# Kernel optimization log

Measured on AMD Instinct MI355X. Metric: run time of the kernel, lower is better.

The kernel has to match this reference:

```python
import jax, jax.numpy as jnp
import numpy as np

N_HEADS = 16
KV_HEADS = 4
HEAD_DIM = 128
D_MODEL = N_HEADS * HEAD_DIM  # 2048
KV_DIM = KV_HEADS * HEAD_DIM  # 512
MAX_POS = 4096
ROPE_THETA = 10000.0
EPS = 1e-5


def _rope_cache(seq_len):
    # QEffMolmoRotaryEmbedding: inv_freq over head_dim, emb = cat(freqs, freqs)
    inv_freq = 1.0 / (ROPE_THETA ** (jnp.arange(0, HEAD_DIM, 2, dtype=jnp.float32) / HEAD_DIM))
    t = jnp.arange(seq_len, dtype=jnp.float32)
    freqs = jnp.outer(t, inv_freq)                      # [S, D/2]
    emb = jnp.concatenate([freqs, freqs], axis=-1)      # [S, D]
    return jnp.cos(emb), jnp.sin(emb)


def _rotate_half(x):
    # x: [B, H, T, D] -> cat(-x2, x1) with halves along last dim
    x1, x2 = jnp.split(x, 2, axis=-1)
    return jnp.concatenate([-x2, x1], axis=-1)


def _rms_norm(x, w):
    var = jnp.mean(jnp.square(x), axis=-1, keepdims=True)
    return (x * jax.lax.rsqrt(var + EPS)) * w


def setup_inputs() -> dict:
    key = jax.random.key(0)
    ks = jax.random.split(key, 8)
    B, T = 1, 2048
    q = jax.random.normal(ks[0], (B, T, D_MODEL), dtype=jnp.float32)
    k = jax.random.normal(ks[1], (B, T, KV_DIM), dtype=jnp.float32)
    v = jax.random.normal(ks[2], (B, T, KV_DIM), dtype=jnp.float32)
    # causal mask: True means masked (torch.where(mask, -10000, scores))
    attention_mask = jnp.triu(jnp.ones((T, T), dtype=bool), k=1)[None, None]  # [1,1,T,T]
    position_ids = jnp.arange(T, dtype=jnp.int32)[None, :]                    # [B,T]
    q_norm_w = jax.random.normal(ks[3], (D_MODEL,), dtype=jnp.float32) * 0.02 + 1.0
    k_norm_w = jax.random.normal(ks[4], (KV_DIM,), dtype=jnp.float32) * 0.02 + 1.0
    w_out = jax.random.normal(ks[5], (D_MODEL, D_MODEL), dtype=jnp.float32) * (D_MODEL ** -0.5)
    return {"q": q, "k": k, "v": v, "attention_mask": attention_mask,
            "position_ids": position_ids, "q_norm_w": q_norm_w,
            "k_norm_w": k_norm_w, "w_out": w_out}


def reference(q, k, v, attention_mask, position_ids, q_norm_w, k_norm_w, w_out):
    B, T, C = q.shape
    # QK-norm on flat projections
    q = _rms_norm(q, q_norm_w)
    k = _rms_norm(k, k_norm_w)
    # split heads: [B, H, T, D]
    q = q.reshape(B, T, N_HEADS, HEAD_DIM).transpose(0, 2, 1, 3)
    k = k.reshape(B, T, KV_HEADS, HEAD_DIM).transpose(0, 2, 1, 3)
    v = v.reshape(B, T, KV_HEADS, HEAD_DIM).transpose(0, 2, 1, 3)
    # RoPE (rotate_half variant)
    cos_c, sin_c = _rope_cache(MAX_POS)
    cos = cos_c[position_ids][:, None]  # [B,1,T,D]
    sin = sin_c[position_ids][:, None]
    q = q * cos + _rotate_half(q) * sin
    k = k * cos + _rotate_half(k) * sin
    # GQA expand
    rep = N_HEADS // KV_HEADS
    k = jnp.repeat(k, rep, axis=1)
    v = jnp.repeat(v, rep, axis=1)
    scale = 1.0 / np.sqrt(HEAD_DIM)
    scores = jnp.einsum('bhqd,bhkd->bhqk', q, k) * scale  # [B,H,T,T]
    scores = jnp.where(attention_mask, jnp.float32(-10000.0), scores)
    attn = jax.nn.softmax(scores.astype(jnp.float32), axis=-1).astype(q.dtype)
    out = jnp.einsum('bhqk,bhkd->bhqd', attn, v)          # [B,H,T,D]
    out = out.transpose(0, 2, 1, 3).reshape(B, T, C)
    return out @ w_out.T
```

## Files before the change

### kernel.cpp

```cpp
#include <hip/hip_runtime.h>
#include <hip/hip_bf16.h>
#include <math.h>

#define T_SEQ 2048
#define NH 16
#define KVH 4
#define HD 128
#define DM 2048
#define KVD 512

typedef short bf16x8 __attribute__((ext_vector_type(8)));
typedef float f32x4 __attribute__((ext_vector_type(4)));
typedef float f32x16 __attribute__((ext_vector_type(16)));
typedef unsigned int uint2v __attribute__((ext_vector_type(2)));

static __device__ __forceinline__ unsigned short f2bf(float f) {
    unsigned int x = __float_as_uint(f);
    x += 0x7fff + ((x >> 16) & 1);
    return (unsigned short)(x >> 16);
}
static __device__ __forceinline__ float bf2f(unsigned short u) {
    return __uint_as_float(((unsigned int)u) << 16);
}

static __device__ __forceinline__ unsigned int cvtpk(float lo, float hi) {
    unsigned int r;
    asm("v_cvt_pk_bf16_f32 %0, %1, %2" : "=v"(r) : "v"(lo), "v"(hi));
    return r;
}

static __device__ __forceinline__ f32x4 mfma16(bf16x8 a, bf16x8 b, f32x4 c) {
    return __builtin_amdgcn_mfma_f32_16x16x32_bf16(a, b, c, 0, 0, 0);
}
static __device__ __forceinline__ f32x16 mfma32(bf16x8 a, bf16x8 b, f32x16 c) {
    return __builtin_amdgcn_mfma_f32_32x32x16_bf16(a, b, c, 0, 0, 0);
}


__global__ __launch_bounds__(256) void qk_prep(
    const float* __restrict__ q, const float* __restrict__ k,
    const float* __restrict__ qw, const float* __restrict__ kw,
    const int* __restrict__ pos_ids,
    unsigned short* __restrict__ Qb, unsigned short* __restrict__ Ks) {
    __shared__ float qr[DM];
    __shared__ float kr[KVD];
    __shared__ float cosL[64], sinL[64];
    __shared__ float redq[4], redk[4];
    int t = blockIdx.x, tid = threadIdx.x;

    float qs = 0.f, ks = 0.f;
    {
        const float* qp = q + (size_t)t * DM + tid * 8;
        float4 v0 = *(const float4*)(qp);
        float4 v1 = *(const float4*)(qp + 4);
        float* dst = qr + tid * 8;
        dst[0] = v0.x; dst[1] = v0.y; dst[2] = v0.z; dst[3] = v0.w;
        dst[4] = v1.x; dst[5] = v1.y; dst[6] = v1.z; dst[7] = v1.w;
        qs = v0.x * v0.x + v0.y * v0.y + v0.z * v0.z + v0.w * v0.w +
             v1.x * v1.x + v1.y * v1.y + v1.z * v1.z + v1.w * v1.w;
        float2 kv = *(const float2*)(k + (size_t)t * KVD + tid * 2);
        kr[tid * 2] = kv.x; kr[tid * 2 + 1] = kv.y;
        ks = kv.x * kv.x + kv.y * kv.y;
    }
    if (tid < 64) {
        float pos = (float)pos_ids[t];
        float inv = powf(10000.0f, -(float)tid * (1.0f / 64.0f));
        float a = pos * inv;
        cosL[tid] = cosf(a);
        sinL[tid] = sinf(a);
    }
    for (int off = 32; off; off >>= 1) {
        qs += __shfl_down(qs, off);
        ks += __shfl_down(ks, off);
    }
    if ((tid & 63) == 0) { redq[tid >> 6] = qs; redk[tid >> 6] = ks; }
    __syncthreads();
    float qinv = rsqrtf((redq[0] + redq[1] + redq[2] + redq[3]) * (1.0f / DM) + 1e-5f);
    float kinv = rsqrtf((redk[0] + redk[1] + redk[2] + redk[3]) * (1.0f / KVD) + 1e-5f);

    {
        int base = tid * 8;
        int h = base >> 7;
        int d = base & 127;
        bool lo = d < 64;
        int i0 = d & 63;
        int pb = lo ? base + 64 : base - 64;
        #pragma unroll
        for (int j = 0; j < 8; ++j) {
            float xv = qr[base + j] * qinv * qw[base + j];
            float pv = qr[pb + j] * qinv * qw[pb + j];
            float c = cosL[i0 + j];
            float s = sinL[i0 + j];
            float o = lo ? (xv * c - pv * s) : (xv * c + pv * s);
            Qb[((size_t)h * T_SEQ + t) * HD + d + j] = f2bf(o);
        }
    }
    {
        int base = tid * 2;
        int kh = base >> 7;
        int d = base & 127;
        bool lo = d < 64;
        int i0 = d & 63;
        int pb = lo ? base + 64 : base - 64;
        int kt = t >> 5, lq = t & 31;
        #pragma unroll
        for (int j = 0; j < 2; ++j) {
            float xv = kr[base + j] * kinv * kw[base + j];
            float pv = kr[pb + j] * kinv * kw[pb + j];
            float c = cosL[i0 + j];
            float s = sinL[i0 + j];
            float o = lo ? (xv * c - pv * s) : (xv * c + pv * s);
            int dj = d + j;
            int sl = dj >> 4, hi2 = (dj >> 3) & 1, jj = dj & 7;
            size_t oi = ((((size_t)(kh * 64 + kt) * 8 + sl) * 2 + hi2) * 32 + lq) * 8 + jj;
            Ks[oi] = f2bf(o);
        }
    }
}

__global__ __launch_bounds__(256) void v_prep(const float* __restrict__ v,
                                              unsigned short* __restrict__ Vs) {
    __shared__ unsigned short tile[64][80];
    int tb = blockIdx.x;
    int cb = blockIdx.y;
    int tid = threadIdx.x;
    #pragma unroll 4
    for (int rep = 0; rep < 16; ++rep) {
        int e = rep * 256 + tid;
        int r = e >> 6;
        int c = e & 63;
        tile[c][r] = f2bf(v[(size_t)(tb * 64 + r) * KVD + cb * 64 + c]);
    }
    __syncthreads();
    #pragma unroll
    for (int rep = 0; rep < 2; ++rep) {
        int e = rep * 256 + tid;
        int cc = e >> 3, tg = e & 7;
        int cg = cb * 64 + cc;
        int kh = cg >> 7, crow = cg & 127, db = crow >> 5, lq = crow & 31;
        int t0g = tb * 64 + tg * 8;
        int kt = t0g >> 5, tr = t0g & 31, half = tr >> 4, hi2 = (tr >> 3) & 1;
        size_t o = (((((size_t)(kh * 64 + kt) * 2 + half) * 4 + db) * 2 + hi2) * 32 + lq) * 8;
        *(bf16x8*)(Vs + o) = *(const bf16x8*)(&tile[cc][tg * 8]);
    }
}

__global__ __launch_bounds__(256) void w_prep(const float* __restrict__ w,
                                              unsigned short* __restrict__ Wb) {
    size_t idx = ((size_t)blockIdx.x * 256 + threadIdx.x) * 4;
    float4 f = *(const float4*)(w + idx);
    ushort4 o;
    o.x = f2bf(f.x); o.y = f2bf(f.y); o.z = f2bf(f.z); o.w = f2bf(f.w);
    *(ushort4*)(Wb + idx) = o;
}

#define BEXP 20.0f
#define SCALE2 (0.08838834764831845f * 1.4426950408889634f)

#define ATTN_BODY(CUR, NXT)                                                        \
    do {                                                                           \
        const unsigned short* Vt_ = Vbase + (size_t)kt * 4096;                     \
        bf16x8 vb[8];                                                              \
        _Pragma("unroll") for (int x = 0; x < 8; ++x)                              \
            vb[x] = *(const bf16x8*)(Vt_ + x * 512);                               \
        if (kt + 1 < t1) {                                                         \
            const unsigned short* Kn_ = Kbase + (size_t)(kt + 1) * 4096;           \
            _Pragma("unroll") for (int x = 0; x < 8; ++x)                          \
                NXT[x] = *(const bf16x8*)(Kn_ + x * 512);                          \
        }                                                                          \
        f32x16 sa_, sb_;                                                           \
        _Pragma("unroll") for (int r = 0; r < 16; ++r) { sa_[r] = 0.f; sb_[r] = 0.f; } \
        _Pragma("unroll") for (int x = 0; x < 8; x += 2) {                         \
            sa_ = mfma32(CUR[x], qf[x], sa_);                                      \
            sb_ = mfma32(CUR[x + 1], qf[x + 1], sb_);                              \
        }                                                                          \
        float p_[16];                                                              \
        if (kt == nkt - 1) {                                                       \
            int lim = qglob - kt * 32;                                             \
            _Pragma("unroll") for (int r = 0; r < 16; ++r) {                       \
                float e_ = __builtin_amdgcn_exp2f((sa_[r] + sb_[r]) * SCALE2 - BEXP); \
                int off_ = (r & 3) + 8 * (r >> 2) + 4 * hi;                        \
                p_[r] = (off_ <= lim) ? e_ : 0.f;                                  \
                sden4[r & 3] += p_[r];                                             \
            }                                                                      \
        } else {                                                                   \
            _Pragma("unroll") for (int r = 0; r < 16; ++r) {                       \
                p_[r] = __builtin_amdgcn_exp2f((sa_[r] + sb_[r]) * SCALE2 - BEXP); \
                sden4[r & 3] += p_[r];                                             \
            }                                                                      \
        }                                                                          \
        _Pragma("unroll") for (int half = 0; half < 2; ++half) {                   \
            unsigned int a0 = cvtpk(p_[half * 8 + 0], p_[half * 8 + 1]);           \
            unsigned int a1 = cvtpk(p_[half * 8 + 2], p_[half * 8 + 3]);           \
            unsigned int b0 = cvtpk(p_[half * 8 + 4], p_[half * 8 + 5]);           \
            unsigned int b1 = cvtpk(p_[half * 8 + 6], p_[half * 8 + 7]);           \
            uint2v w0 = __builtin_amdgcn_permlane32_swap(a0, b0, false, false);    \
            uint2v w1 = __builtin_amdgcn_permlane32_swap(a1, b1, false, false);    \
            union { unsigned int u[4]; bf16x8 v; } pc;                             \
            pc.u[0] = w0[0]; pc.u[1] = w1[0]; pc.u[2] = w0[1]; pc.u[3] = w1[1];    \
            bf16x8 pf = pc.v;                                                      \
            _Pragma("unroll") for (int db = 0; db < 4; ++db)                       \
                oacc[db] = mfma32(vb[half * 4 + db], pf, oacc[db]);                \
        }                                                                          \
    } while (0)

__global__ __launch_bounds__(64) void attn_fwd11(
    const unsigned short* __restrict__ Qb, const unsigned short* __restrict__ Ks,
    const unsigned short* __restrict__ Vs,
    unsigned short* __restrict__ Opart, float* __restrict__ Lpart,
    unsigned short* __restrict__ Xo, int CHUNK) {
    int qrow = 63 - (int)blockIdx.x;
    int h = blockIdx.y;
    int seg = blockIdx.z;
    int kh = h >> 2;
    int l = threadIdx.x;
    int lq = l & 31, hi = l >> 5;
    int qglob = qrow * 32 + lq;

    int nkt = qrow + 1;
    int t0 = seg * CHUNK;
    int t1 = min(t0 + CHUNK, nkt);
    if (t0 >= t1) return;
    size_t idx = (size_t)(h * 64 + qrow) * 4 + seg;

    const unsigned short* Qh = Qb + (size_t)h * T_SEQ * HD;
    const unsigned short* Kbase = Ks + (size_t)kh * 64 * 4096 + l * 8;
    const unsigned short* Vbase = Vs + (size_t)kh * 64 * 4096 + l * 8;

    bf16x8 qf[8];
    #pragma unroll
    for (int sl = 0; sl < 8; ++sl)
        qf[sl] = *(const bf16x8*)(Qh + (size_t)qglob * HD + sl * 16 + hi * 8);

    f32x16 oacc[4];
    #pragma unroll
    for (int db = 0; db < 4; ++db)
        #pragma unroll
        for (int r = 0; r < 16; ++r) oacc[db][r] = 0.f;
    f32x4 sden4 = (f32x4){0.f, 0.f, 0.f, 0.f};

    bf16x8 kA[8], kB[8];
    {
        const unsigned short* K0 = Kbase + (size_t)t0 * 4096;
        #pragma unroll
        for (int x = 0; x < 8; ++x) kA[x] = *(const bf16x8*)(K0 + x * 512);
    }
    int kt = t0;
    while (true) {
        ATTN_BODY(kA, kB);
        if (++kt >= t1) break;
        ATTN_BODY(kB, kA);
        if (++kt >= t1) break;
    }

    float sden = (sden4[0] + sden4[1]) + (sden4[2] + sden4[3]);
    float sden_tot = sden + __shfl_xor(sden, 32);

    if (t0 == 0 && t1 == nkt) {
        float invs = 1.0f / sden_tot;
        #pragma unroll
        for (int db = 0; db < 4; ++db) {
            #pragma unroll
            for (int r = 0; r < 16; ++r) {
                int d = db * 32 + (r & 3) + 8 * (r >> 2) + 4 * hi;
                Xo[(size_t)qglob * DM + h * HD + d] = f2bf(oacc[db][r] * invs);
            }
        }
        return;
    }
    if (hi == 0) Lpart[idx * 32 + lq] = sden_tot;
    unsigned short* op = Opart + (idx << 12);
    #pragma unroll
    for (int db = 0; db < 4; ++db) {
        #pragma unroll
        for (int r = 0; r < 16; ++r) {
            int d = db * 32 + (r & 3) + 8 * (r >> 2) + 4 * hi;
            op[d * 32 + lq] = f2bf(oacc[db][r]);
        }
    }
}

__global__ __launch_bounds__(256) void attn_combine(
    const unsigned short* __restrict__ Opart, const float* __restrict__ Lpart,
    unsigned short* __restrict__ Xo, int CHUNK) {
    int qrow = CHUNK + blockIdx.x;
    int h = blockIdx.y;
    int tid = threadIdx.x;
    int nkt = qrow + 1;
    int used = (nkt + CHUNK - 1) / CHUNK;
    int base = (h * 64 + qrow) * 4;
    __shared__ float invden[32];
    if (tid < 32) {
        int q = tid;
        float den = 0.f;
        for (int s = 0; s < used; ++s) den += Lpart[(base + s) * 32 + q];
        invden[q] = 1.0f / den;
    }
    __syncthreads();
    int d = tid >> 1, q0 = (tid & 1) * 16;
    float acc[16];
    #pragma unroll
    for (int j = 0; j < 16; ++j) acc[j] = 0.f;
    for (int s = 0; s < used; ++s) {
        const unsigned short* op = Opart + ((size_t)(base + s) << 12) + d * 32 + q0;
        bf16x8 o0 = *(const bf16x8*)(op);
        bf16x8 o1 = *(const bf16x8*)(op + 8);
        #pragma unroll
        for (int j = 0; j < 8; ++j) {
            acc[j]     += bf2f((unsigned short)o0[j]);
            acc[8 + j] += bf2f((unsigned short)o1[j]);
        }
    }
    __shared__ unsigned short xo[32][136];
    #pragma unroll
    for (int j = 0; j < 16; ++j)
        xo[q0 + j][d] = f2bf(acc[j] * invden[q0 + j]);
    __syncthreads();
    int q = tid >> 3, dc = (tid & 7) * 16;
    bf16x8 v0 = *(const bf16x8*)(&xo[q][dc]);
    bf16x8 v1 = *(const bf16x8*)(&xo[q][dc + 8]);
    size_t ro = (size_t)(qrow * 32 + q) * DM + h * HD + dc;
    *(bf16x8*)(Xo + ro) = v0;
    *(bf16x8*)(Xo + ro + 8) = v1;
}

__global__ __launch_bounds__(256) void outproj2(
    const unsigned short* __restrict__ X, const unsigned short* __restrict__ Wb,
    float* __restrict__ out) {
    __shared__ unsigned short As[128][72];
    __shared__ unsigned short Bs[64][72];
    int tid = threadIdx.x;
    int w = tid >> 6, l = tid & 63;
    int lr = l & 15, lg = l >> 4;
    int wm = w >> 1, wn = w & 1;
    int id = blockIdx.x;
    int wg = (id & 7) * 64 + (id >> 3);
    int m0 = (wg & 15) * 128, n0 = (wg >> 4) * 64;

    int ar_row[4], ar_col[4], br_row[2], br_col[2];
    #pragma unroll
    for (int qd = 0; qd < 4; ++qd) {
        int c = tid + qd * 256;
        ar_row[qd] = c >> 3; ar_col[qd] = (c & 7) * 8;
    }
    #pragma unroll
    for (int qd = 0; qd < 2; ++qd) {
        int c = tid + qd * 256;
        br_row[qd] = c >> 3; br_col[qd] = (c & 7) * 8;
    }

    f32x4 acc[4][2];
    #pragma unroll
    for (int i = 0; i < 4; ++i)
        #pragma unroll
        for (int j = 0; j < 2; ++j) acc[i][j] = (f32x4){0.f, 0.f, 0.f, 0.f};

    bf16x8 ar[4], br[2];
    #pragma unroll
    for (int qd = 0; qd < 4; ++qd)
        ar[qd] = *(const bf16x8*)(X + (size_t)(m0 + ar_row[qd]) * DM + ar_col[qd]);
    #pragma unroll
    for (int qd = 0; qd < 2; ++qd)
        br[qd] = *(const bf16x8*)(Wb + (size_t)(n0 + br_row[qd]) * DM + br_col[qd]);
    #pragma unroll
    for (int qd = 0; qd < 4; ++qd)
        *(bf16x8*)(&As[ar_row[qd]][ar_col[qd]]) = ar[qd];
    #pragma unroll
    for (int qd = 0; qd < 2; ++qd)
        *(bf16x8*)(&Bs[br_row[qd]][br_col[qd]]) = br[qd];
    __syncthreads();

    for (int t = 0; t < DM / 64; ++t) {
        if (t + 1 < DM / 64) {
            int k0 = (t + 1) * 64;
            #pragma unroll
            for (int qd = 0; qd < 4; ++qd)
                ar[qd] = *(const bf16x8*)(X + (size_t)(m0 + ar_row[qd]) * DM + k0 + ar_col[qd]);
            #pragma unroll
            for (int qd = 0; qd < 2; ++qd)
                br[qd] = *(const bf16x8*)(Wb + (size_t)(n0 + br_row[qd]) * DM + k0 + br_col[qd]);
        }
        #pragma unroll
        for (int ks = 0; ks < 2; ++ks) {
            bf16x8 af[4], bfr[2];
            #pragma unroll
            for (int i = 0; i < 4; ++i)
                af[i] = *(const bf16x8*)(&As[wm * 64 + i * 16 + lr][ks * 32 + lg * 8]);
            #pragma unroll
            for (int j = 0; j < 2; ++j)
                bfr[j] = *(const bf16x8*)(&Bs[wn * 32 + j * 16 + lr][ks * 32 + lg * 8]);
            #pragma unroll
            for (int i = 0; i < 4; ++i)
                #pragma unroll
                for (int j = 0; j < 2; ++j)
                    acc[i][j] = mfma16(af[i], bfr[j], acc[i][j]);
        }
        if (t + 1 < DM / 64) {
            __syncthreads();
            #pragma unroll
            for (int qd = 0; qd < 4; ++qd)
                *(bf16x8*)(&As[ar_row[qd]][ar_col[qd]]) = ar[qd];
            #pragma unroll
            for (int qd = 0; qd < 2; ++qd)
                *(bf16x8*)(&Bs[br_row[qd]][br_col[qd]]) = br[qd];
            __syncthreads();
        }
    }
    #pragma unroll
    for (int i = 0; i < 4; ++i) {
        #pragma unroll
        for (int j = 0; j < 2; ++j) {
            #pragma unroll
            for (int r = 0; r < 4; ++r) {
                int row = m0 + wm * 64 + i * 16 + lg * 4 + r;
                int col = n0 + wn * 32 + j * 16 + lr;
                out[(size_t)row * DM + col] = acc[i][j][r];
            }
        }
    }
}

extern "C" void kernel_launch(void* const* d_in, const int* in_sizes, int n_in,
                              void* d_out, int out_size, void* d_ws, size_t ws_size,
                              hipStream_t stream) {
    const float* q = (const float*)d_in[0];
    const float* k = (const float*)d_in[1];
    const float* v = (const float*)d_in[2];
    const int* pos_ids = (const int*)d_in[4];
    const float* qw = (const float*)d_in[5];
    const float* kw = (const float*)d_in[6];
    const float* wout = (const float*)d_in[7];
    float* out = (float*)d_out;

    char* ws = (char*)d_ws;
    unsigned short* Qb = (unsigned short*)(ws + 0x100000);
    unsigned short* Ks = (unsigned short*)(ws + 0x900000);
    unsigned short* Vs = (unsigned short*)(ws + 0xB00000);
    unsigned short* Wb = (unsigned short*)(ws + 0xD00000);
    unsigned short* Xo = (unsigned short*)(ws + 0x1500000);
    float* Lpart = (float*)(ws + 0x1D00000);
    unsigned short* Opart = (unsigned short*)(ws + 0x1E00000);

    int CHUNK = (ws_size >= 0x1E00000ull + 4ull * 0x800000ull) ? 22 : 64;
    int zsegs = (CHUNK == 22) ? 3 : 1;

    qk_prep<<<T_SEQ, 256, 0, stream>>>(q, k, qw, kw, pos_ids, Qb, Ks);
    v_prep<<<dim3(T_SEQ / 64, KVD / 64), 256, 0, stream>>>(v, Vs);
    w_prep<<<(DM * DM) / (256 * 4), 256, 0, stream>>>(wout, Wb);
    attn_fwd11<<<dim3(64, NH, zsegs), 64, 0, stream>>>(Qb, Ks, Vs, Opart, Lpart, Xo, CHUNK);
    if (CHUNK == 22)
        attn_combine<<<dim3(64 - 22, NH), 256, 0, stream>>>(Opart, Lpart, Xo, CHUNK);
    outproj2<<<512, 256, 0, stream>>>(Xo, Wb, out);
}
```

Baseline: 99.93 us.

## Share K/V tiles across GQA heads via LDS with async double-buffered loads

The attention kernel now runs one 256-thread block per KV head, with four waves each handling one of the query heads in the group. Each K/V tile is loaded once into shared memory with global_load_lds, where previously each query head's wave fetched it separately from global memory. The next tile is prefetched into a double buffer. This cuts redundant global/L2 traffic by the GQA factor, but adds a __syncthreads per tile, reads operands from LDS, and launches a quarter as many blocks.

```diff
diff --git a/kernel.cpp b/kernel.cpp
--- a/kernel.cpp
+++ b/kernel.cpp
@@ -34,6 +34,13 @@
 }
 static __device__ __forceinline__ f32x16 mfma32(bf16x8 a, bf16x8 b, f32x16 c) {
     return __builtin_amdgcn_mfma_f32_32x32x16_bf16(a, b, c, 0, 0, 0);
+}
+
+static __device__ __forceinline__ void gl_lds16(const unsigned short* g, unsigned short* l) {
+    __builtin_amdgcn_global_load_lds(
+        (const __attribute__((address_space(1))) unsigned int*)g,
+        (__attribute__((address_space(3))) unsigned int*)l,
+        16, 0, 0);
 }
 
 
@@ -157,63 +164,27 @@
 #define BEXP 20.0f
 #define SCALE2 (0.08838834764831845f * 1.4426950408889634f)
 
-#define ATTN_BODY(CUR, NXT)                                                        \
+#define STAGE(B, KT)                                                               \
     do {                                                                           \
-        const unsigned short* Vt_ = Vbase + (size_t)kt * 4096;                     \
-        bf16x8 vb[8];                                                              \
-        _Pragma("unroll") for (int x = 0; x < 8; ++x)                              \
-            vb[x] = *(const bf16x8*)(Vt_ + x * 512);                               \
-        if (kt + 1 < t1) {                                                         \
-            const unsigned short* Kn_ = Kbase + (size_t)(kt + 1) * 4096;           \
-            _Pragma("unroll") for (int x = 0; x < 8; ++x)                          \
-                NXT[x] = *(const bf16x8*)(Kn_ + x * 512);                          \
-        }                                                                          \
-        f32x16 sa_, sb_;                                                           \
-        _Pragma("unroll") for (int r = 0; r < 16; ++r) { sa_[r] = 0.f; sb_[r] = 0.f; } \
-        _Pragma("unroll") for (int x = 0; x < 8; x += 2) {                         \
-            sa_ = mfma32(CUR[x], qf[x], sa_);                                      \
-            sb_ = mfma32(CUR[x + 1], qf[x + 1], sb_);                              \
-        }                                                                          \
-        float p_[16];                                                              \
-        if (kt == nkt - 1) {                                                       \
-            int lim = qglob - kt * 32;                                             \
-            _Pragma("unroll") for (int r = 0; r < 16; ++r) {                       \
-                float e_ = __builtin_amdgcn_exp2f((sa_[r] + sb_[r]) * SCALE2 - BEXP); \
-                int off_ = (r & 3) + 8 * (r >> 2) + 4 * hi;                        \
-                p_[r] = (off_ <= lim) ? e_ : 0.f;                                  \
-                sden4[r & 3] += p_[r];                                             \
-            }                                                                      \
-        } else {                                                                   \
-            _Pragma("unroll") for (int r = 0; r < 16; ++r) {                       \
-                p_[r] = __builtin_amdgcn_exp2f((sa_[r] + sb_[r]) * SCALE2 - BEXP); \
-                sden4[r & 3] += p_[r];                                             \
-            }                                                                      \
-        }                                                                          \
-        _Pragma("unroll") for (int half = 0; half < 2; ++half) {                   \
-            unsigned int a0 = cvtpk(p_[half * 8 + 0], p_[half * 8 + 1]);           \
-            unsigned int a1 = cvtpk(p_[half * 8 + 2], p_[half * 8 + 3]);           \
-            unsigned int b0 = cvtpk(p_[half * 8 + 4], p_[half * 8 + 5]);           \
-            unsigned int b1 = cvtpk(p_[half * 8 + 6], p_[half * 8 + 7]);           \
-            uint2v w0 = __builtin_amdgcn_permlane32_swap(a0, b0, false, false);    \
-            uint2v w1 = __builtin_amdgcn_permlane32_swap(a1, b1, false, false);    \
-            union { unsigned int u[4]; bf16x8 v; } pc;                             \
-            pc.u[0] = w0[0]; pc.u[1] = w1[0]; pc.u[2] = w0[1]; pc.u[3] = w1[1];    \
-            bf16x8 pf = pc.v;                                                      \
-            _Pragma("unroll") for (int db = 0; db < 4; ++db)                       \
-                oacc[db] = mfma32(vb[half * 4 + db], pf, oacc[db]);                \
-        }                                                                          \
+        const unsigned short* kg_ = Kt_g + (size_t)(KT) * 4096;                    \
+        const unsigned short* vg_ = Vt_g + (size_t)(KT) * 4096;                    \
+        gl_lds16(kg_ + w * 512 + l * 8,        &kv[B][w * 512]);                   \
+        gl_lds16(kg_ + 2048 + w * 512 + l * 8, &kv[B][2048 + w * 512]);            \
+        gl_lds16(vg_ + w * 512 + l * 8,        &kv[B][4096 + w * 512]);            \
+        gl_lds16(vg_ + 2048 + w * 512 + l * 8, &kv[B][6144 + w * 512]);            \
     } while (0)
 
-__global__ __launch_bounds__(64) void attn_fwd11(
+__global__ __launch_bounds__(256) void attn_fwd12(
     const unsigned short* __restrict__ Qb, const unsigned short* __restrict__ Ks,
     const unsigned short* __restrict__ Vs,
     unsigned short* __restrict__ Opart, float* __restrict__ Lpart,
     unsigned short* __restrict__ Xo, int CHUNK) {
     int qrow = 63 - (int)blockIdx.x;
-    int h = blockIdx.y;
+    int kh = blockIdx.y;
     int seg = blockIdx.z;
-    int kh = h >> 2;
-    int l = threadIdx.x;
+    int tid = threadIdx.x;
+    int w = tid >> 6, l = tid & 63;
+    int h = kh * 4 + w;
     int lq = l & 31, hi = l >> 5;
     int qglob = qrow * 32 + lq;
 
@@ -224,8 +195,10 @@
     size_t idx = (size_t)(h * 64 + qrow) * 4 + seg;
 
     const unsigned short* Qh = Qb + (size_t)h * T_SEQ * HD;
-    const unsigned short* Kbase = Ks + (size_t)kh * 64 * 4096 + l * 8;
-    const unsigned short* Vbase = Vs + (size_t)kh * 64 * 4096 + l * 8;
+    const unsigned short* Kt_g = Ks + (size_t)kh * 64 * 4096;
+    const unsigned short* Vt_g = Vs + (size_t)kh * 64 * 4096;
+
+    __shared__ unsigned short kv[2][8192];
 
     bf16x8 qf[8];
     #pragma unroll
@@ -239,18 +212,58 @@
         for (int r = 0; r < 16; ++r) oacc[db][r] = 0.f;
     f32x4 sden4 = (f32x4){0.f, 0.f, 0.f, 0.f};
 
-    bf16x8 kA[8], kB[8];
-    {
-        const unsigned short* K0 = Kbase + (size_t)t0 * 4096;
-        #pragma unroll
-        for (int x = 0; x < 8; ++x) kA[x] = *(const bf16x8*)(K0 + x * 512);
-    }
-    int kt = t0;
-    while (true) {
-        ATTN_BODY(kA, kB);
-        if (++kt >= t1) break;
-        ATTN_BODY(kB, kA);
-        if (++kt >= t1) break;
+    STAGE(0, t0);
+    int cur = 0;
+    for (int kt = t0; kt < t1; ++kt) {
+        __syncthreads();
+        if (kt + 1 < t1) STAGE(cur ^ 1, kt + 1);
+        const unsigned short* kl = &kv[cur][0] + l * 8;
+        const unsigned short* vl = &kv[cur][4096] + l * 8;
+        f32x16 sa, sb;
+        #pragma unroll
+        for (int r = 0; r < 16; ++r) { sa[r] = 0.f; sb[r] = 0.f; }
+        #pragma unroll
+        for (int x = 0; x < 8; x += 2) {
+            bf16x8 k0 = *(const bf16x8*)(kl + x * 512);
+            bf16x8 k1 = *(const bf16x8*)(kl + (x + 1) * 512);
+            sa = mfma32(k0, qf[x], sa);
+            sb = mfma32(k1, qf[x + 1], sb);
+        }
+        float p_[16];
+        if (kt == nkt - 1) {
+            int lim = qglob - kt * 32;
+            #pragma unroll
+            for (int r = 0; r < 16; ++r) {
+                float e_ = __builtin_amdgcn_exp2f((sa[r] + sb[r]) * SCALE2 - BEXP);
+                int off_ = (r & 3) + 8 * (r >> 2) + 4 * hi;
+                p_[r] = (off_ <= lim) ? e_ : 0.f;
+                sden4[r & 3] += p_[r];
+            }
+        } else {
+            #pragma unroll
+            for (int r = 0; r < 16; ++r) {
+                p_[r] = __builtin_amdgcn_exp2f((sa[r] + sb[r]) * SCALE2 - BEXP);
+                sden4[r & 3] += p_[r];
+            }
+        }
+        #pragma unroll
+        for (int half = 0; half < 2; ++half) {
+            unsigned int a0 = cvtpk(p_[half * 8 + 0], p_[half * 8 + 1]);
+            unsigned int a1 = cvtpk(p_[half * 8 + 2], p_[half * 8 + 3]);
+            unsigned int b0 = cvtpk(p_[half * 8 + 4], p_[half * 8 + 5]);
+            unsigned int b1 = cvtpk(p_[half * 8 + 6], p_[half * 8 + 7]);
+            uint2v w0 = __builtin_amdgcn_permlane32_swap(a0, b0, false, false);
+            uint2v w1 = __builtin_amdgcn_permlane32_swap(a1, b1, false, false);
+            union { unsigned int u[4]; bf16x8 v; } pc;
+            pc.u[0] = w0[0]; pc.u[1] = w1[0]; pc.u[2] = w0[1]; pc.u[3] = w1[1];
+            bf16x8 pf = pc.v;
+            #pragma unroll
+            for (int db = 0; db < 4; ++db) {
+                bf16x8 vf = *(const bf16x8*)(vl + (half * 4 + db) * 512);
+                oacc[db] = mfma32(vf, pf, oacc[db]);
+            }
+        }
+        cur ^= 1;
     }
 
     float sden = (sden4[0] + sden4[1]) + (sden4[2] + sden4[3]);
@@ -447,7 +460,7 @@
     qk_prep<<<T_SEQ, 256, 0, stream>>>(q, k, qw, kw, pos_ids, Qb, Ks);
     v_prep<<<dim3(T_SEQ / 64, KVD / 64), 256, 0, stream>>>(v, Vs);
     w_prep<<<(DM * DM) / (256 * 4), 256, 0, stream>>>(wout, Wb);
-    attn_fwd11<<<dim3(64, NH, zsegs), 64, 0, stream>>>(Qb, Ks, Vs, Opart, Lpart, Xo, CHUNK);
+    attn_fwd12<<<dim3(64, KVH, zsegs), 256, 0, stream>>>(Qb, Ks, Vs, Opart, Lpart, Xo, CHUNK);
     if (CHUNK == 22)
         attn_combine<<<dim3(64 - 22, NH), 256, 0, stream>>>(Opart, Lpart, Xo, CHUNK);
     outproj2<<<512, 256, 0, stream>>>(Xo, Wb, out);
```

Result: faster. 95.62 us (-4.3%).

## Share K/V tiles across GQA heads via LDS with async double-buffered loads

Applied to the files above, without the earlier changes.

The attention kernel now runs one 256-thread block per KV head, with four waves, one per query head in the group. Each K/V tile is loaded once into LDS with global_load_lds and double-buffered in pairs, instead of every head's wave reading the same K/V from global memory. The V and W conversion kernels are also merged into one launch. This cuts redundant K/V global traffic and one kernel launch, at the cost of barriers, more LDS per block (64 KB), and a quarter as many blocks, which may lower occupancy.

```diff
diff --git a/kernel.cpp b/kernel.cpp
--- a/kernel.cpp
+++ b/kernel.cpp
@@ -34,6 +34,13 @@
 }
 static __device__ __forceinline__ f32x16 mfma32(bf16x8 a, bf16x8 b, f32x16 c) {
     return __builtin_amdgcn_mfma_f32_32x32x16_bf16(a, b, c, 0, 0, 0);
+}
+
+static __device__ __forceinline__ void gl_lds16(const unsigned short* g, unsigned short* l) {
+    __builtin_amdgcn_global_load_lds(
+        (const __attribute__((address_space(1))) unsigned int*)g,
+        (__attribute__((address_space(3))) unsigned int*)l,
+        16, 0, 0);
 }
 
 
@@ -118,12 +125,24 @@
     }
 }
 
-__global__ __launch_bounds__(256) void v_prep(const float* __restrict__ v,
-                                              unsigned short* __restrict__ Vs) {
+__global__ __launch_bounds__(256) void vw_prep(const float* __restrict__ v,
+                                               unsigned short* __restrict__ Vs,
+                                               const float* __restrict__ w,
+                                               unsigned short* __restrict__ Wb) {
+    int bid = blockIdx.x;
+    int tid = threadIdx.x;
+    if (bid < 4096) {
+        size_t idx = ((size_t)bid * 256 + tid) * 4;
+        float4 f = *(const float4*)(w + idx);
+        ushort4 o;
+        o.x = f2bf(f.x); o.y = f2bf(f.y); o.z = f2bf(f.z); o.w = f2bf(f.w);
+        *(ushort4*)(Wb + idx) = o;
+        return;
+    }
     __shared__ unsigned short tile[64][80];
-    int tb = blockIdx.x;
-    int cb = blockIdx.y;
-    int tid = threadIdx.x;
+    int vb = bid - 4096;
+    int tb = vb & 31;
+    int cb = vb >> 5;
     #pragma unroll 4
     for (int rep = 0; rep < 16; ++rep) {
         int e = rep * 256 + tid;
@@ -145,47 +164,43 @@
     }
 }
 
-__global__ __launch_bounds__(256) void w_prep(const float* __restrict__ w,
-                                              unsigned short* __restrict__ Wb) {
-    size_t idx = ((size_t)blockIdx.x * 256 + threadIdx.x) * 4;
-    float4 f = *(const float4*)(w + idx);
-    ushort4 o;
-    o.x = f2bf(f.x); o.y = f2bf(f.y); o.z = f2bf(f.z); o.w = f2bf(f.w);
-    *(ushort4*)(Wb + idx) = o;
-}
-
 #define BEXP 20.0f
 #define SCALE2 (0.08838834764831845f * 1.4426950408889634f)
 
-#define ATTN_BODY(CUR, NXT)                                                        \
+#define STAGE1(B, S, KT)                                                           \
     do {                                                                           \
-        const unsigned short* Vt_ = Vbase + (size_t)kt * 4096;                     \
-        bf16x8 vb[8];                                                              \
-        _Pragma("unroll") for (int x = 0; x < 8; ++x)                              \
-            vb[x] = *(const bf16x8*)(Vt_ + x * 512);                               \
-        if (kt + 1 < t1) {                                                         \
-            const unsigned short* Kn_ = Kbase + (size_t)(kt + 1) * 4096;           \
-            _Pragma("unroll") for (int x = 0; x < 8; ++x)                          \
-                NXT[x] = *(const bf16x8*)(Kn_ + x * 512);                          \
-        }                                                                          \
-        f32x16 sa_, sb_;                                                           \
-        _Pragma("unroll") for (int r = 0; r < 16; ++r) { sa_[r] = 0.f; sb_[r] = 0.f; } \
+        const unsigned short* kg_ = Kt_g + (size_t)(KT) * 4096;                    \
+        const unsigned short* vg_ = Vt_g + (size_t)(KT) * 4096;                    \
+        gl_lds16(kg_ + w * 512 + l * 8,        &kv[B][S][w * 512]);                \
+        gl_lds16(kg_ + 2048 + w * 512 + l * 8, &kv[B][S][2048 + w * 512]);         \
+        gl_lds16(vg_ + w * 512 + l * 8,        &kv[B][S][4096 + w * 512]);         \
+        gl_lds16(vg_ + 2048 + w * 512 + l * 8, &kv[B][S][6144 + w * 512]);         \
+    } while (0)
+
+#define TILE_COMPUTE(BUF, SLOT, KT)                                                \
+    do {                                                                           \
+        const unsigned short* kl = &kv[BUF][SLOT][0] + l * 8;                      \
+        const unsigned short* vl = &kv[BUF][SLOT][4096] + l * 8;                   \
+        f32x16 sa, sb;                                                             \
+        _Pragma("unroll") for (int r = 0; r < 16; ++r) { sa[r] = 0.f; sb[r] = 0.f; } \
         _Pragma("unroll") for (int x = 0; x < 8; x += 2) {                         \
-            sa_ = mfma32(CUR[x], qf[x], sa_);                                      \
-            sb_ = mfma32(CUR[x + 1], qf[x + 1], sb_);                              \
+            bf16x8 k0 = *(const bf16x8*)(kl + x * 512);                            \
+            bf16x8 k1 = *(const bf16x8*)(kl + (x + 1) * 512);                      \
+            sa = mfma32(k0, qf[x], sa);                                            \
+            sb = mfma32(k1, qf[x + 1], sb);                                        \
         }                                                                          \
         float p_[16];                                                              \
-        if (kt == nkt - 1) {                                                       \
-            int lim = qglob - kt * 32;                                             \
+        if ((KT) == nkt - 1) {                                                     \
+            int lim = qglob - (KT) * 32;                                           \
             _Pragma("unroll") for (int r = 0; r < 16; ++r) {                       \
-                float e_ = __builtin_amdgcn_exp2f((sa_[r] + sb_[r]) * SCALE2 - BEXP); \
+                float e_ = __builtin_amdgcn_exp2f((sa[r] + sb[r]) * SCALE2 - BEXP); \
                 int off_ = (r & 3) + 8 * (r >> 2) + 4 * hi;                        \
                 p_[r] = (off_ <= lim) ? e_ : 0.f;                                  \
                 sden4[r & 3] += p_[r];                                             \
             }                                                                      \
         } else {                                                                   \
             _Pragma("unroll") for (int r = 0; r < 16; ++r) {                       \
-                p_[r] = __builtin_amdgcn_exp2f((sa_[r] + sb_[r]) * SCALE2 - BEXP); \
+                p_[r] = __builtin_amdgcn_exp2f((sa[r] + sb[r]) * SCALE2 - BEXP);   \
                 sden4[r & 3] += p_[r];                                             \
             }                                                                      \
         }                                                                          \
@@ -199,21 +214,24 @@
             union { unsigned int u[4]; bf16x8 v; } pc;                             \
             pc.u[0] = w0[0]; pc.u[1] = w1[0]; pc.u[2] = w0[1]; pc.u[3] = w1[1];    \
             bf16x8 pf = pc.v;                                                      \
-            _Pragma("unroll") for (int db = 0; db < 4; ++db)                       \
-                oacc[db] = mfma32(vb[half * 4 + db], pf, oacc[db]);                \
+            _Pragma("unroll") for (int db = 0; db < 4; ++db) {                     \
+                bf16x8 vf = *(const bf16x8*)(vl + (half * 4 + db) * 512);          \
+                oacc[db] = mfma32(vf, pf, oacc[db]);                               \
+            }                                                                      \
         }                                                                          \
     } while (0)
 
-__global__ __launch_bounds__(64) void attn_fwd11(
+__global__ __launch_bounds__(256) void attn_fwd18(
     const unsigned short* __restrict__ Qb, const unsigned short* __restrict__ Ks,
     const unsigned short* __restrict__ Vs,
     unsigned short* __restrict__ Opart, float* __restrict__ Lpart,
     unsigned short* __restrict__ Xo, int CHUNK) {
     int qrow = 63 - (int)blockIdx.x;
-    int h = blockIdx.y;
+    int kh = blockIdx.y;
     int seg = blockIdx.z;
-    int kh = h >> 2;
-    int l = threadIdx.x;
+    int tid = threadIdx.x;
+    int w = tid >> 6, l = tid & 63;
+    int h = kh * 4 + w;
     int lq = l & 31, hi = l >> 5;
     int qglob = qrow * 32 + lq;
 
@@ -224,8 +242,10 @@
     size_t idx = (size_t)(h * 64 + qrow) * 4 + seg;
 
     const unsigned short* Qh = Qb + (size_t)h * T_SEQ * HD;
-    const unsigned short* Kbase = Ks + (size_t)kh * 64 * 4096 + l * 8;
-    const unsigned short* Vbase = Vs + (size_t)kh * 64 * 4096 + l * 8;
+    const unsigned short* Kt_g = Ks + (size_t)kh * 64 * 4096;
+    const unsigned short* Vt_g = Vs + (size_t)kh * 64 * 4096;
+
+    __shared__ unsigned short kv[2][2][8192];
 
     bf16x8 qf[8];
     #pragma unroll
@@ -239,18 +259,28 @@
         for (int r = 0; r < 16; ++r) oacc[db][r] = 0.f;
     f32x4 sden4 = (f32x4){0.f, 0.f, 0.f, 0.f};
 
-    bf16x8 kA[8], kB[8];
-    {
-        const unsigned short* K0 = Kbase + (size_t)t0 * 4096;
-        #pragma unroll
-        for (int x = 0; x < 8; ++x) kA[x] = *(const bf16x8*)(K0 + x * 512);
-    }
+    int pairsEnd = t0 + ((t1 - t0) & ~1);
     int kt = t0;
-    while (true) {
-        ATTN_BODY(kA, kB);
-        if (++kt >= t1) break;
-        ATTN_BODY(kB, kA);
-        if (++kt >= t1) break;
+    int cur = 0;
+    if (kt < pairsEnd) { STAGE1(0, 0, kt); STAGE1(0, 1, kt + 1); }
+    if (kt + 2 < pairsEnd) { STAGE1(1, 0, kt + 2); STAGE1(1, 1, kt + 3); }
+    for (; kt < pairsEnd; kt += 2) {
+        bool more = (kt + 2 < pairsEnd);
+        if (more) asm volatile("s_waitcnt vmcnt(8)" ::: "memory");
+        else      asm volatile("s_waitcnt vmcnt(0)" ::: "memory");
+        __builtin_amdgcn_s_barrier();
+        TILE_COMPUTE(cur, 0, kt);
+        TILE_COMPUTE(cur, 1, kt + 1);
+        asm volatile("s_waitcnt lgkmcnt(0)" ::: "memory");
+        __builtin_amdgcn_s_barrier();
+        if (kt + 4 < pairsEnd) { STAGE1(cur, 0, kt + 4); STAGE1(cur, 1, kt + 5); }
+        cur ^= 1;
+    }
+    if (kt < t1) {
+        STAGE1(cur, 0, kt);
+        asm volatile("s_waitcnt vmcnt(0)" ::: "memory");
+        __builtin_amdgcn_s_barrier();
+        TILE_COMPUTE(cur, 0, kt);
     }
 
     float sden = (sden4[0] + sden4[1]) + (sden4[2] + sden4[3]);
@@ -445,9 +475,8 @@
     int zsegs = (CHUNK == 22) ? 3 : 1;
 
     qk_prep<<<T_SEQ, 256, 0, stream>>>(q, k, qw, kw, pos_ids, Qb, Ks);
-    v_prep<<<dim3(T_SEQ / 64, KVD / 64), 256, 0, stream>>>(v, Vs);
-    w_prep<<<(DM * DM) / (256 * 4), 256, 0, stream>>>(wout, Wb);
-    attn_fwd11<<<dim3(64, NH, zsegs), 64, 0, stream>>>(Qb, Ks, Vs, Opart, Lpart, Xo, CHUNK);
+    vw_prep<<<4096 + 256, 256, 0, stream>>>(v, Vs, wout, Wb);
+    attn_fwd18<<<dim3(64, KVH, zsegs), 256, 0, stream>>>(Qb, Ks, Vs, Opart, Lpart, Xo, CHUNK);
     if (CHUNK == 22)
         attn_combine<<<dim3(64 - 22, NH), 256, 0, stream>>>(Opart, Lpart, Xo, CHUNK);
     outproj2<<<512, 256, 0, stream>>>(Xo, Wb, out);
```

Measured after the change: 93.82 us. 6.1% less time.
